# Performance work log

Measured on AMD Instinct MI355X. Metric: run time of the kernel, lower is better.

The kernel has to match this reference:

```python
import jax, jax.numpy as jnp
import numpy as np


def _pixel_unshuffle(y, r=2):
    # torch.nn.PixelUnshuffle: out[:, c*r*r + i*r + j, h, w] = in[:, c, h*r+i, w*r+j]
    B, C, H, W = y.shape
    y = y.reshape(B, C, H // r, r, W // r, r)
    y = y.transpose(0, 1, 3, 5, 2, 4)  # (B, C, r, r, H//r, W//r)
    return y.reshape(B, C * r * r, H // r, W // r)


def setup_inputs() -> dict:
    key = jax.random.key(0)
    kx, kw = jax.random.split(key)
    n_feat = 96
    x = jax.random.normal(kx, (8, n_feat, 256, 256), dtype=jnp.float32)
    # conv weight: (out=n_feat//2, in=n_feat, 3, 3), kaiming-ish scale
    fan_in = n_feat * 3 * 3
    W = jax.random.normal(kw, (n_feat // 2, n_feat, 3, 3), dtype=jnp.float32) * (1.0 / np.sqrt(fan_in))
    return {"x": x, "W": W}


def reference(x, W):
    # 3x3 conv, stride 1, padding 1, no bias (FP32 path of QConv2ds)
    y = jax.lax.conv_general_dilated(
        x, W,
        window_strides=(1, 1),
        padding=((1, 1), (1, 1)),
        dimension_numbers=("NCHW", "OIHW", "NCHW"),
    )
    # PixelUnshuffle(2): [B, C/2, H, W] -> [B, 2C, H/2, W/2]
    return _pixel_unshuffle(y, r=2)
```

## Files before the change

kernel.cpp:

```cpp
#include <hip/hip_runtime.h>
#include <hip/hip_bf16.h>


typedef __attribute__((ext_vector_type(8))) short bf16x8;
typedef __attribute__((ext_vector_type(4))) float f32x4;
typedef __attribute__((ext_vector_type(4))) unsigned uint4v;

#define CIN 96
#define COUT 48
#define HW 256
#define WTH 4
#define WTW 16
#define WHH (WTH + 2)
#define WHW (WTW + 2)
#define WNP (WHH * WHW)
#define CC 32
#define CIPAD 40

static __device__ __forceinline__ unsigned bfbits(float f) {
    unsigned u = __builtin_bit_cast(unsigned, f);
    return (u + 0x7fffu + ((u >> 16) & 1u)) >> 16;
}
static __device__ __forceinline__ unsigned packbf(float lo, float hi) {
    __hip_bfloat162 h = __float22bfloat162_rn(float2{lo, hi});
    unsigned r;
    __builtin_memcpy(&r, &h, sizeof(r));
    return r;
}

__global__ __launch_bounds__(256) void wtransform(
    const float* __restrict__ Wg, short* __restrict__ blob)
{
    int t = blockIdx.x * 256 + threadIdx.x;
    if (t >= COUT * CIN * 9) return;
    int co  = t / (CIN * 9);
    int rem = t - co * (CIN * 9);
    int ci  = rem / 9;
    int d   = rem - ci * 9;
    int cc  = ci >> 5, cl = ci & 31;
    int ct  = co >> 4;
    int lane = (co & 15) | ((cl >> 3) << 4);
    int j   = cl & 7;
    blob[((((cc * 9 + d) * 3 + ct) * 64 + lane) * 8) + j] = (short)bfbits(Wg[t]);
}

__global__ __launch_bounds__(256, 4) void conv3x3_unshuffle_mfma(
    const float* __restrict__ x,
    const short* __restrict__ wblob,
    float* __restrict__ out)
{
    __shared__ short xs[4][WNP * CIPAD];

    const int tid  = threadIdx.x;
    const int lane = tid & 63;
    const int wv   = tid >> 6;

    int bid = blockIdx.x;
    int nid = (bid & 7) * 256 + (bid >> 3);
    int b   = nid >> 8;
    int ty  = (nid >> 4) & 15;
    int tx  = nid & 15;
    int h0  = ty * 16 + wv * WTH;
    int w0  = tx * 16;

    const float* xb = x + (size_t)b * CIN * HW * HW;
    short* xw = xs[wv];

    f32x4 acc[WTH][3];
#pragma unroll
    for (int pt = 0; pt < WTH; ++pt)
#pragma unroll
        for (int ct = 0; ct < 3; ++ct)
            acc[pt][ct] = (f32x4){0.f, 0.f, 0.f, 0.f};

    bf16x8 afc[3];
#pragma unroll
    for (int ct = 0; ct < 3; ++ct)
        afc[ct] = *(const bf16x8*)(wblob + ct * 512 + lane * 8);

    for (int cc = 0; cc < CIN / CC; ++cc) {
#pragma unroll
        for (int cig = 0; cig < 4; ++cig) {
#pragma unroll
            for (int rep = 0; rep < 2; ++rep) {
                int p = lane + rep * 64;
                bool act = p < WNP;
                int r = p / WHW;
                int c = p - r * WHW;
                int gh = h0 + r - 1;
                int gw = w0 + c - 1;
                float v[8];
#pragma unroll
                for (int j = 0; j < 8; ++j) v[j] = 0.f;
                if (act & ((unsigned)gh < HW) & ((unsigned)gw < HW)) {
                    const float* src = xb + (size_t)(cc * CC + cig * 8) * HW * HW
                                          + gh * HW + gw;
#pragma unroll
                    for (int j = 0; j < 8; ++j) v[j] = src[(size_t)j * HW * HW];
                }
                if (act) {
                    uint4v pk;
                    pk.x = packbf(v[0], v[1]);
                    pk.y = packbf(v[2], v[3]);
                    pk.z = packbf(v[4], v[5]);
                    pk.w = packbf(v[6], v[7]);
                    *(uint4v*)&xw[p * CIPAD + cig * 8] = pk;
                }
            }
        }

        const short* wc = wblob + (size_t)cc * 9 * 3 * 512;
#pragma unroll
        for (int d = 0; d < 9; ++d) {
            const short* wn = (d < 8) ? (wc + (d + 1) * 3 * 512)
                                      : (cc < 2 ? wc + 9 * 3 * 512 : wc);
            bf16x8 afn[3];
#pragma unroll
            for (int ct = 0; ct < 3; ++ct)
                afn[ct] = *(const bf16x8*)(wn + ct * 512 + lane * 8);

            const int dy = d / 3, dx = d - 3 * (d / 3);
            bf16x8 bfv[WTH];
#pragma unroll
            for (int pt = 0; pt < WTH; ++pt) {
                int hr = pt + dy;
                int hc = (lane & 15) + dx;
                bfv[pt] = *(const bf16x8*)&xw[(hr * WHW + hc) * CIPAD + (lane >> 4) * 8];
            }
#pragma unroll
            for (int pt = 0; pt < WTH; ++pt)
#pragma unroll
                for (int ct = 0; ct < 3; ++ct)
                    acc[pt][ct] = __builtin_amdgcn_mfma_f32_16x16x32_bf16(
                        afc[ct], bfv[pt], acc[pt][ct], 0, 0, 0);
#pragma unroll
            for (int ct = 0; ct < 3; ++ct) afc[ct] = afn[ct];
        }
    }

#pragma unroll
    for (int pt = 0; pt < WTH; ++pt) {
        int oh = h0 + pt;
        int ow = w0 + (lane & 15);
        int sub = ((oh & 1) << 1) | (ow & 1);
        size_t pixoff = (size_t)(oh >> 1) * (HW / 2) + (ow >> 1);
#pragma unroll
        for (int ct = 0; ct < 3; ++ct) {
#pragma unroll
            for (int e = 0; e < 4; ++e) {
                int co = ct * 16 + (lane >> 4) * 4 + e;
                out[((size_t)b * (COUT * 4) + co * 4 + sub) * (HW / 2) * (HW / 2) + pixoff] =
                    acc[pt][ct][e];
            }
        }
    }
}

extern "C" void kernel_launch(void* const* d_in, const int* in_sizes, int n_in,
                              void* d_out, int out_size, void* d_ws, size_t ws_size,
                              hipStream_t stream) {
    const float* x  = (const float*)d_in[0];
    const float* Wg = (const float*)d_in[1];
    float* out      = (float*)d_out;
    short* blob     = (short*)d_ws;

    wtransform<<<(COUT * CIN * 9 + 255) / 256, 256, 0, stream>>>(Wg, blob);

    conv3x3_unshuffle_mfma<<<dim3(2048), dim3(256), 0, stream>>>(x, blob, out);
}
```

Baseline: 388.6 us.

## Stage input halo via direct global-to-LDS loads with block-shared fp32 tile

Replaces per-wave register loads with fp32-to-bf16 packing by 16-byte global_load_lds transfers of fp32 runs into a block-shared LDS tile, with a rotated column layout to spread bank accesses. Conversion to bf16 now happens when reading MFMA operands from LDS. Tiles become 4x32 per block, shared by all four waves instead of per-wave 4x16, which cuts redundant halo loads. The grid doubles and occupancy is raised to 5 blocks. The cost is extra LDS reads and packing per MFMA step, plus block-wide barriers. Halo columns narrower than a 4-float run near the edges are handled by zero-fill and bounds checks.

```diff
diff --git a/kernel.cpp b/kernel.cpp
--- a/kernel.cpp
+++ b/kernel.cpp
@@ -6,16 +6,20 @@
 typedef __attribute__((ext_vector_type(4))) float f32x4;
 typedef __attribute__((ext_vector_type(4))) unsigned uint4v;
 
+typedef const __attribute__((address_space(1))) void GV;
+typedef __attribute__((address_space(3))) void LV;
+
 #define CIN 96
 #define COUT 48
 #define HW 256
-#define WTH 4
-#define WTW 16
-#define WHH (WTH + 2)
-#define WHW (WTW + 2)
-#define WNP (WHH * WHW)
+#define TH 4
+#define TW 32
+#define HR 6
+#define HCW 40
+#define NRUN 10
 #define CC 32
-#define CIPAD 40
+#define NTASK (CC * HR * NRUN)
+#define NSLOT 2048
 
 static __device__ __forceinline__ unsigned bfbits(float f) {
     unsigned u = __builtin_bit_cast(unsigned, f);
@@ -44,31 +48,36 @@
     blob[((((cc * 9 + d) * 3 + ct) * 64 + lane) * 8) + j] = (short)bfbits(Wg[t]);
 }
 
-__global__ __launch_bounds__(256, 4) void conv3x3_unshuffle_mfma(
+__global__ __launch_bounds__(256, 5) void conv3x3_unshuffle_mfma(
     const float* __restrict__ x,
     const short* __restrict__ wblob,
     float* __restrict__ out)
 {
-    __shared__ short xs[4][WNP * CIPAD];
+    __shared__ float xs[NSLOT * 4];
 
     const int tid  = threadIdx.x;
     const int lane = tid & 63;
     const int wv   = tid >> 6;
 
     int bid = blockIdx.x;
-    int nid = (bid & 7) * 256 + (bid >> 3);
-    int b   = nid >> 8;
-    int ty  = (nid >> 4) & 15;
-    int tx  = nid & 15;
-    int h0  = ty * 16 + wv * WTH;
-    int w0  = tx * 16;
+    int b   = bid & 7;
+    int t0  = bid >> 3;
+    int ty  = ((t0 >> 6) << 3) | ((t0 >> 3) & 7);
+    int tx  = t0 & 7;
+    int h0  = ty * TH;
+    int w0  = tx * TW;
 
     const float* xb = x + (size_t)b * CIN * HW * HW;
-    short* xw = xs[wv];
 
-    f32x4 acc[WTH][3];
+    if (ty == 0 || ty == 63 || tx == 0 || tx == 7) {
+        for (int i = tid; i < NSLOT; i += 256)
+            *(uint4v*)&xs[i * 4] = (uint4v){0u, 0u, 0u, 0u};
+        __syncthreads();
+    }
+
+    f32x4 acc[2][3];
 #pragma unroll
-    for (int pt = 0; pt < WTH; ++pt)
+    for (int pt = 0; pt < 2; ++pt)
 #pragma unroll
         for (int ct = 0; ct < 3; ++ct)
             acc[pt][ct] = (f32x4){0.f, 0.f, 0.f, 0.f};
@@ -80,34 +89,24 @@
 
     for (int cc = 0; cc < CIN / CC; ++cc) {
 #pragma unroll
-        for (int cig = 0; cig < 4; ++cig) {
-#pragma unroll
-            for (int rep = 0; rep < 2; ++rep) {
-                int p = lane + rep * 64;
-                bool act = p < WNP;
-                int r = p / WHW;
-                int c = p - r * WHW;
-                int gh = h0 + r - 1;
-                int gw = w0 + c - 1;
-                float v[8];
-#pragma unroll
-                for (int j = 0; j < 8; ++j) v[j] = 0.f;
-                if (act & ((unsigned)gh < HW) & ((unsigned)gw < HW)) {
-                    const float* src = xb + (size_t)(cc * CC + cig * 8) * HW * HW
-                                          + gh * HW + gw;
-#pragma unroll
-                    for (int j = 0; j < 8; ++j) v[j] = src[(size_t)j * HW * HW];
-                }
-                if (act) {
-                    uint4v pk;
-                    pk.x = packbf(v[0], v[1]);
-                    pk.y = packbf(v[2], v[3]);
-                    pk.z = packbf(v[4], v[5]);
-                    pk.w = packbf(v[6], v[7]);
-                    *(uint4v*)&xw[p * CIPAD + cig * 8] = pk;
-                }
-            }
+        for (int k = 0; k < 8; ++k) {
+            int t   = tid + k * 256;
+            int ci  = t / 60;
+            int rem = t - ci * 60;
+            int r   = rem / 10;
+            int rp  = rem - r * 10;
+            int kg  = ci >> 3;
+            int run = rp - 2 * kg; if (run < 0) run += 10;
+            int gh  = h0 + r - 1;
+            int gw0 = w0 - 4 + run * 4;
+            bool ok = (t < NTASK) & ((unsigned)gh < HW) & ((unsigned)gw0 < (HW - 3));
+            const float* src = xb + (((size_t)(cc * CC + ci)) << 16)
+                                  + (gh << 8) + gw0;
+            if (ok)
+                __builtin_amdgcn_global_load_lds((GV*)src,
+                    (LV*)(xs + (size_t)(k * 256 + wv * 64) * 4), 16, 0, 0);
         }
+        __syncthreads();
 
         const short* wc = wblob + (size_t)cc * 9 * 3 * 512;
 #pragma unroll
@@ -119,16 +118,27 @@
             for (int ct = 0; ct < 3; ++ct)
                 afn[ct] = *(const bf16x8*)(wn + ct * 512 + lane * 8);
 
-            const int dy = d / 3, dx = d - 3 * (d / 3);
-            bf16x8 bfv[WTH];
+            const int dy = d / 3, dx = d - 3 * dy;
+            const int r  = wv + dy;
+            const int kg = lane >> 4;
+            bf16x8 bfv[2];
 #pragma unroll
-            for (int pt = 0; pt < WTH; ++pt) {
-                int hr = pt + dy;
-                int hc = (lane & 15) + dx;
-                bfv[pt] = *(const bf16x8*)&xw[(hr * WHW + hc) * CIPAD + (lane >> 4) * 8];
+            for (int pt = 0; pt < 2; ++pt) {
+                int c  = pt * 16 + (lane & 15) + dx + 3;
+                int c2 = c + 8 * kg; if (c2 >= HCW) c2 -= HCW;
+                float f[8];
+#pragma unroll
+                for (int j = 0; j < 8; ++j)
+                    f[j] = xs[((8 * kg + j) * 6 + r) * 40 + c2];
+                uint4v pk;
+                pk.x = packbf(f[0], f[1]);
+                pk.y = packbf(f[2], f[3]);
+                pk.z = packbf(f[4], f[5]);
+                pk.w = packbf(f[6], f[7]);
+                __builtin_memcpy(&bfv[pt], &pk, 16);
             }
 #pragma unroll
-            for (int pt = 0; pt < WTH; ++pt)
+            for (int pt = 0; pt < 2; ++pt)
 #pragma unroll
                 for (int ct = 0; ct < 3; ++ct)
                     acc[pt][ct] = __builtin_amdgcn_mfma_f32_16x16x32_bf16(
@@ -136,12 +146,13 @@
 #pragma unroll
             for (int ct = 0; ct < 3; ++ct) afc[ct] = afn[ct];
         }
+        if (cc < 2) __syncthreads();
     }
 
+    const int oh = h0 + wv;
 #pragma unroll
-    for (int pt = 0; pt < WTH; ++pt) {
-        int oh = h0 + pt;
-        int ow = w0 + (lane & 15);
+    for (int pt = 0; pt < 2; ++pt) {
+        int ow = w0 + pt * 16 + (lane & 15);
         int sub = ((oh & 1) << 1) | (ow & 1);
         size_t pixoff = (size_t)(oh >> 1) * (HW / 2) + (ow >> 1);
 #pragma unroll
@@ -166,5 +177,5 @@
 
     wtransform<<<(COUT * CIN * 9 + 255) / 256, 256, 0, stream>>>(Wg, blob);
 
-    conv3x3_unshuffle_mfma<<<dim3(2048), dim3(256), 0, stream>>>(x, blob, out);
+    conv3x3_unshuffle_mfma<<<dim3(4096), dim3(256), 0, stream>>>(x, blob, out);
 }
```

Result: slower. 416.8 us (+7.3%).
